# Kernel optimization log

Hardware: AMD Instinct MI355X
Metric: run time of the kernel (lower is better)

Reference implementation:

```python
import jax, jax.numpy as jnp
import numpy as np

NUM_EMBEDDINGS = 8192
EMBEDDING_DIM = 256
PROJECTION_DIM = 128


def setup_inputs() -> dict:
    key = jax.random.key(0)
    k_x, k_cb, k_w, k_b = jax.random.split(key, 4)
    x = jax.random.normal(k_x, (16, 1024, EMBEDDING_DIM), dtype=jnp.float32)
    codebook = jax.random.normal(k_cb, (NUM_EMBEDDINGS, EMBEDDING_DIM), dtype=jnp.float32)
    proj_w = jax.random.normal(k_w, (EMBEDDING_DIM, PROJECTION_DIM), dtype=jnp.float32) / np.sqrt(EMBEDDING_DIM)
    proj_b = jax.random.normal(k_b, (PROJECTION_DIM,), dtype=jnp.float32) * 0.01
    return {"x": x, "codebook": codebook, "proj_w": proj_w, "proj_b": proj_b}


def reference(x, codebook, proj_w, proj_b):
    # Flatten tokens: [N, D]
    x_flat = x.reshape(-1, EMBEDDING_DIM)
    # Project tokens and codebook into the distance space: [N, P], [K, P]
    x_proj = x_flat @ proj_w + proj_b
    cb_proj = codebook @ proj_w + proj_b
    # Squared euclidean distances via expansion: [N, K]
    distances = (
        jnp.sum(x_proj ** 2, axis=1, keepdims=True)
        - 2.0 * (x_proj @ cb_proj.T)
        + jnp.sum(cb_proj ** 2, axis=1)
    )
    idx = jnp.argmin(distances, axis=1)
    discrete = jax.nn.one_hot(idx, NUM_EMBEDDINGS, dtype=x.dtype)  # [N, K]
    # One-hot matmul lookup (disguised gather): [N, D]
    quantized = (discrete @ codebook).reshape(x.shape)
    return (discrete, quantized)
```

## Files before the change

kernel.cpp:

```cpp
#include <hip/hip_runtime.h>
#include <math.h>

#define D 256
#define P 128
#define K 8192
#define NTOK 16384
#define NROWS (NTOK + K)
#define NCHUNK 8
#define KCHUNK (K / NCHUNK)
#define CAPC 128
#define MARGIN 3.0f
#define FLT_BIG 3.402823466e+38f

typedef __attribute__((ext_vector_type(8))) short bf16x8;
typedef __attribute__((ext_vector_type(4))) float f32x4;
typedef __attribute__((ext_vector_type(8))) unsigned short u16x8;

__device__ __forceinline__ unsigned short f32_to_bf16_rne(float f) {
    unsigned int u = __float_as_uint(f);
    u = (u + 0x7fffu + ((u >> 16) & 1u)) >> 16;
    return (unsigned short)u;
}

__global__ __launch_bounds__(256) void zero_kernel(float4* __restrict__ p, size_t n4) {
    size_t i = (size_t)blockIdx.x * blockDim.x + threadIdx.x;
    size_t stride = (size_t)gridDim.x * blockDim.x;
    float4 z; z.x = 0.f; z.y = 0.f; z.z = 0.f; z.w = 0.f;
    for (; i < n4; i += stride) p[i] = z;
}

__global__ __launch_bounds__(256) void proj_kernel(
    const float* __restrict__ x, const float* __restrict__ cb,
    const float* __restrict__ w, const float* __restrict__ bias,
    float* __restrict__ xproj, float* __restrict__ cproj,
    float* __restrict__ xnorm, float* __restrict__ cnorm,
    unsigned short* __restrict__ xh, unsigned short* __restrict__ chs,
    unsigned long long* __restrict__ best, int* __restrict__ cnt)
{
    __shared__ float As[16][D];
    const int tid = threadIdx.x;
    const int row0 = blockIdx.x * 16;

    {
        int g = blockIdx.x * 256 + tid;
        if (g < NTOK) { best[g] = 0xFFFFFFFFFFFFFFFFull; cnt[g] = 0; }
    }

    for (int i = tid; i < 16 * (D / 4); i += 256) {
        int r = i / (D / 4);
        int c4 = i % (D / 4);
        int gr = row0 + r;
        const float* src = (gr < NTOK) ? (x + (size_t)gr * D)
                                       : (cb + (size_t)(gr - NTOK) * D);
        float4 v = ((const float4*)src)[c4];
        ((float4*)&As[r][0])[c4] = v;
    }
    __syncthreads();

    const int r = tid >> 4;
    const int c0 = (tid & 15) * 8;

    float acc[8];
#pragma unroll
    for (int j = 0; j < 8; j++) acc[j] = 0.f;

    for (int d = 0; d < D; d += 4) {
        float4 a4 = *(const float4*)&As[r][d];
#pragma unroll
        for (int dd = 0; dd < 4; dd++) {
            float av = (dd == 0) ? a4.x : (dd == 1) ? a4.y : (dd == 2) ? a4.z : a4.w;
            float4 w0 = *(const float4*)&w[(size_t)(d + dd) * P + c0];
            float4 w1 = *(const float4*)&w[(size_t)(d + dd) * P + c0 + 4];
            acc[0] = fmaf(av, w0.x, acc[0]);
            acc[1] = fmaf(av, w0.y, acc[1]);
            acc[2] = fmaf(av, w0.z, acc[2]);
            acc[3] = fmaf(av, w0.w, acc[3]);
            acc[4] = fmaf(av, w1.x, acc[4]);
            acc[5] = fmaf(av, w1.y, acc[5]);
            acc[6] = fmaf(av, w1.z, acc[6]);
            acc[7] = fmaf(av, w1.w, acc[7]);
        }
    }

    float out[8];
    float nrm = 0.f;
    u16x8 hv;
#pragma unroll
    for (int j = 0; j < 8; j++) {
        out[j] = acc[j] + bias[c0 + j];
        nrm = fmaf(out[j], out[j], nrm);
        hv[j] = f32_to_bf16_rne(out[j]);
    }

    const int gr = row0 + r;
    if (gr < NTOK) {
        float* dst = xproj + (size_t)gr * P;
        float4 o0; o0.x = out[0]; o0.y = out[1]; o0.z = out[2]; o0.w = out[3];
        float4 o1; o1.x = out[4]; o1.y = out[5]; o1.z = out[6]; o1.w = out[7];
        *(float4*)&dst[c0] = o0;
        *(float4*)&dst[c0 + 4] = o1;
        *(u16x8*)(xh + (size_t)gr * P + c0) = hv;
    } else {
        int row = gr - NTOK;
        float* dst = cproj + (size_t)row * P;
        float4 o0; o0.x = out[0]; o0.y = out[1]; o0.z = out[2]; o0.w = out[3];
        float4 o1; o1.x = out[4]; o1.y = out[5]; o1.z = out[6]; o1.w = out[7];
        *(float4*)&dst[c0] = o0;
        *(float4*)&dst[c0 + 4] = o1;
        int t64 = row >> 6, rg = (row >> 4) & 3, l15 = row & 15;
        int ks = c0 >> 5, quad = (c0 >> 3) & 3;
        size_t atom = ((size_t)(t64 * 16 + rg * 4 + ks) * 4 + quad) * 16 + l15;
        *(u16x8*)(chs + atom * 8) = hv;
    }

#pragma unroll
    for (int off = 1; off < 16; off <<= 1)
        nrm += __shfl_xor(nrm, off, 16);
    if ((tid & 15) == 0) {
        if (gr < NTOK) xnorm[gr] = nrm;
        else           cnorm[gr - NTOK] = nrm;
    }
}

__global__ __launch_bounds__(256) void filter_kernel(
    const unsigned short* __restrict__ xh, const unsigned short* __restrict__ chs,
    const float* __restrict__ xnorm, const float* __restrict__ cnorm,
    int* __restrict__ cnt, int* __restrict__ cand)
{
    const int tid = threadIdx.x;
    const int tok0 = blockIdx.x * 128;
    const int k0 = blockIdx.y * KCHUNK;

    const int wave = tid >> 6;
    const int lane = tid & 63;
    const int quad = lane >> 4;
    const int l15 = lane & 15;

    bf16x8 afrag[2][4];
#pragma unroll
    for (int mi = 0; mi < 2; mi++)
#pragma unroll
        for (int ks = 0; ks < 4; ks++)
            afrag[mi][ks] = *(const bf16x8*)(
                xh + (size_t)(tok0 + wave * 32 + mi * 16 + l15) * P + ks * 32 + quad * 8);

    float xnv[2][4];
#pragma unroll
    for (int mi = 0; mi < 2; mi++)
#pragma unroll
        for (int r = 0; r < 4; r++)
            xnv[mi][r] = xnorm[tok0 + wave * 32 + mi * 16 + quad * 4 + r];

    float rmin[2][4];
#pragma unroll
    for (int mi = 0; mi < 2; mi++)
#pragma unroll
        for (int r = 0; r < 4; r++) rmin[mi][r] = FLT_BIG;

    for (int ct = 0; ct < KCHUNK / 64; ct++) {
        const int kt = k0 + ct * 64;
        const int t64 = kt >> 6;

        f32x4 acc[2][4];
#pragma unroll
        for (int mi = 0; mi < 2; mi++)
#pragma unroll
            for (int nj = 0; nj < 4; nj++)
                acc[mi][nj] = (f32x4)(0.f);

#pragma unroll
        for (int ks = 0; ks < 4; ks++) {
            const bf16x8* base = (const bf16x8*)(chs) + (size_t)(t64 * 16 + ks) * 64 + lane;
            bf16x8 b0 = base[0 * 4 * 64];
            bf16x8 b1 = base[1 * 4 * 64];
            bf16x8 b2 = base[2 * 4 * 64];
            bf16x8 b3 = base[3 * 4 * 64];
            acc[0][0] = __builtin_amdgcn_mfma_f32_16x16x32_bf16(afrag[0][ks], b0, acc[0][0], 0, 0, 0);
            acc[0][1] = __builtin_amdgcn_mfma_f32_16x16x32_bf16(afrag[0][ks], b1, acc[0][1], 0, 0, 0);
            acc[0][2] = __builtin_amdgcn_mfma_f32_16x16x32_bf16(afrag[0][ks], b2, acc[0][2], 0, 0, 0);
            acc[0][3] = __builtin_amdgcn_mfma_f32_16x16x32_bf16(afrag[0][ks], b3, acc[0][3], 0, 0, 0);
            acc[1][0] = __builtin_amdgcn_mfma_f32_16x16x32_bf16(afrag[1][ks], b0, acc[1][0], 0, 0, 0);
            acc[1][1] = __builtin_amdgcn_mfma_f32_16x16x32_bf16(afrag[1][ks], b1, acc[1][1], 0, 0, 0);
            acc[1][2] = __builtin_amdgcn_mfma_f32_16x16x32_bf16(afrag[1][ks], b2, acc[1][2], 0, 0, 0);
            acc[1][3] = __builtin_amdgcn_mfma_f32_16x16x32_bf16(afrag[1][ks], b3, acc[1][3], 0, 0, 0);
        }

        float cn[4];
#pragma unroll
        for (int nj = 0; nj < 4; nj++) cn[nj] = cnorm[kt + nj * 16 + l15];

#pragma unroll
        for (int mi = 0; mi < 2; mi++)
#pragma unroll
            for (int r = 0; r < 4; r++) {
                float d[4];
#pragma unroll
                for (int nj = 0; nj < 4; nj++)
                    d[nj] = (xnv[mi][r] - 2.0f * acc[mi][nj][r]) + cn[nj];
                float m = fminf(fminf(d[0], d[1]), fminf(d[2], d[3]));
#pragma unroll
                for (int off = 1; off < 16; off <<= 1)
                    m = fminf(m, __shfl_xor(m, off));
                float rm = fminf(rmin[mi][r], m);
                rmin[mi][r] = rm;
                float thr = rm + MARGIN;
                const int tok = tok0 + wave * 32 + mi * 16 + quad * 4 + r;
#pragma unroll
                for (int nj = 0; nj < 4; nj++) {
                    if (d[nj] <= thr) {
                        int pos = atomicAdd(&cnt[tok], 1);
                        if (pos < CAPC) cand[(size_t)tok * CAPC + pos] = kt + nj * 16 + l15;
                    }
                }
            }
    }
}

__global__ __launch_bounds__(256) void rescore_kernel(
    const float* __restrict__ xproj, const float* __restrict__ cproj,
    const float* __restrict__ xnorm, const float* __restrict__ cnorm,
    const int* __restrict__ cnt, const int* __restrict__ cand,
    unsigned long long* __restrict__ best)
{
    const int tid = threadIdx.x;
    const int lane = tid & 63;
    const int wave = tid >> 6;
    const int t = blockIdx.x * 4 + wave;

    int n = cnt[t];
    if (n > CAPC) n = CAPC;
    const float xn = xnorm[t];
    const float* xr = xproj + (size_t)t * P;

    for (int j = lane; j < n; j += 64) {
        int k = cand[(size_t)t * CAPC + j];
        const float* cr = cproj + (size_t)k * P;
        float s = 0.f;
#pragma unroll 8
        for (int p = 0; p < P; p += 4) {
            float4 a = *(const float4*)&xr[p];
            float4 b = *(const float4*)&cr[p];
            s = fmaf(a.x, b.x, s);
            s = fmaf(a.y, b.y, s);
            s = fmaf(a.z, b.z, s);
            s = fmaf(a.w, b.w, s);
        }
        float dist = (xn - 2.0f * s) + cnorm[k];
        unsigned long long pack =
            ((unsigned long long)__float_as_uint(dist) << 32) |
            (unsigned long long)(unsigned)k;
        atomicMin(&best[t], pack);
    }
}

__global__ __launch_bounds__(256) void finalize_kernel(
    const unsigned long long* __restrict__ best, const float* __restrict__ cb,
    float* __restrict__ discrete, float* __restrict__ quant)
{
    __shared__ int sidx[64];
    const int tid = threadIdx.x;
    const int tok0 = blockIdx.x * 64;

    if (tid < 64) {
        int t = tok0 + tid;
        int bi = (int)(best[t] & 0xFFFFFFFFull);
        sidx[tid] = bi;
        discrete[(size_t)t * K + bi] = 1.0f;
    }
    __syncthreads();

    for (int i = tid; i < 64 * (D / 4); i += 256) {
        int t = i >> 6;
        int c4 = i & 63;
        int bi = sidx[t];
        float4 v = ((const float4*)(cb + (size_t)bi * D))[c4];
        ((float4*)(quant + (size_t)(tok0 + t) * D))[c4] = v;
    }
}

extern "C" void kernel_launch(void* const* d_in, const int* in_sizes, int n_in,
                              void* d_out, int out_size, void* d_ws, size_t ws_size,
                              hipStream_t stream) {
    const float* x    = (const float*)d_in[0];
    const float* cb   = (const float*)d_in[1];
    const float* w    = (const float*)d_in[2];
    const float* bias = (const float*)d_in[3];

    float* out = (float*)d_out;
    float* discrete = out;
    float* quant = out + (size_t)NTOK * K;

    char* ws = (char*)d_ws;
    size_t off = 0;
    float* xproj = (float*)(ws + off); off += (size_t)NTOK * P * 4;
    float* cproj = (float*)(ws + off); off += (size_t)K * P * 4;
    float* xnorm = (float*)(ws + off); off += (size_t)NTOK * 4;
    float* cnorm = (float*)(ws + off); off += (size_t)K * 4;
    unsigned short* xh  = (unsigned short*)(ws + off); off += (size_t)NTOK * P * 2;
    unsigned short* chs = (unsigned short*)(ws + off); off += (size_t)K * P * 2;
    int* cnt  = (int*)(ws + off); off += (size_t)NTOK * 4;
    int* cand = (int*)(ws + off); off += (size_t)NTOK * CAPC * 4;
    unsigned long long* best = (unsigned long long*)(ws + off); off += (size_t)NTOK * 8;

    zero_kernel<<<dim3(8192), dim3(256), 0, stream>>>(
        (float4*)discrete, (size_t)NTOK * K / 4);

    proj_kernel<<<dim3(NROWS / 16), dim3(256), 0, stream>>>(
        x, cb, w, bias, xproj, cproj, xnorm, cnorm, xh, chs, best, cnt);

    filter_kernel<<<dim3(NTOK / 128, NCHUNK), dim3(256), 0, stream>>>(
        xh, chs, xnorm, cnorm, cnt, cand);

    rescore_kernel<<<dim3(NTOK / 4), dim3(256), 0, stream>>>(
        xproj, cproj, xnorm, cnorm, cnt, cand, best);

    finalize_kernel<<<dim3(NTOK / 64), dim3(256), 0, stream>>>(
        best, cb, discrete, quant);
}
```

Baseline: 969.5 us.

## Fuse one-hot zeroing into filter kernel and merge rescore with finalize

```diff
diff --git a/kernel.cpp b/kernel.cpp
--- a/kernel.cpp
+++ b/kernel.cpp
@@ -22,20 +22,13 @@
     return (unsigned short)u;
 }
 
-__global__ __launch_bounds__(256) void zero_kernel(float4* __restrict__ p, size_t n4) {
-    size_t i = (size_t)blockIdx.x * blockDim.x + threadIdx.x;
-    size_t stride = (size_t)gridDim.x * blockDim.x;
-    float4 z; z.x = 0.f; z.y = 0.f; z.z = 0.f; z.w = 0.f;
-    for (; i < n4; i += stride) p[i] = z;
-}
-
 __global__ __launch_bounds__(256) void proj_kernel(
     const float* __restrict__ x, const float* __restrict__ cb,
     const float* __restrict__ w, const float* __restrict__ bias,
     float* __restrict__ xproj, float* __restrict__ cproj,
     float* __restrict__ xnorm, float* __restrict__ cnorm,
     unsigned short* __restrict__ xh, unsigned short* __restrict__ chs,
-    unsigned long long* __restrict__ best, int* __restrict__ cnt)
+    int* __restrict__ cnt)
 {
     __shared__ float As[16][D];
     const int tid = threadIdx.x;
@@ -43,7 +36,7 @@
 
     {
         int g = blockIdx.x * 256 + tid;
-        if (g < NTOK) { best[g] = 0xFFFFFFFFFFFFFFFFull; cnt[g] = 0; }
+        if (g < NTOK) cnt[g] = 0;
     }
 
     for (int i = tid; i < 16 * (D / 4); i += 256) {
@@ -122,20 +115,25 @@
     }
 }
 
-__global__ __launch_bounds__(256) void filter_kernel(
+__global__ __launch_bounds__(256) void filterz_kernel(
     const unsigned short* __restrict__ xh, const unsigned short* __restrict__ chs,
     const float* __restrict__ xnorm, const float* __restrict__ cnorm,
-    int* __restrict__ cnt, int* __restrict__ cand)
+    int* __restrict__ cnt, int* __restrict__ cand,
+    float* __restrict__ discrete)
 {
     const int tid = threadIdx.x;
     const int tok0 = blockIdx.x * 128;
     const int k0 = blockIdx.y * KCHUNK;
+    const int flat = blockIdx.y * gridDim.x + blockIdx.x;
 
     const int wave = tid >> 6;
     const int lane = tid & 63;
     const int quad = lane >> 4;
     const int l15 = lane & 15;
 
+    f32x4* zbase = (f32x4*)discrete + (size_t)flat * 32768;
+    const f32x4 zv = (f32x4)(0.f);
+
     bf16x8 afrag[2][4];
 #pragma unroll
     for (int mi = 0; mi < 2; mi++)
@@ -160,6 +158,10 @@
     for (int ct = 0; ct < KCHUNK / 64; ct++) {
         const int kt = k0 + ct * 64;
         const int t64 = kt >> 6;
+
+#pragma unroll
+        for (int s = 0; s < 8; s++)
+            zbase[(size_t)ct * 2048 + s * 256 + tid] = zv;
 
         f32x4 acc[2][4];
 #pragma unroll
@@ -216,56 +218,56 @@
     }
 }
 
-__global__ __launch_bounds__(256) void rescore_kernel(
+__global__ __launch_bounds__(256) void rescorefinal_kernel(
     const float* __restrict__ xproj, const float* __restrict__ cproj,
     const float* __restrict__ xnorm, const float* __restrict__ cnorm,
     const int* __restrict__ cnt, const int* __restrict__ cand,
-    unsigned long long* __restrict__ best)
-{
-    const int tid = threadIdx.x;
-    const int lane = tid & 63;
-    const int wave = tid >> 6;
-    const int t = blockIdx.x * 4 + wave;
-
-    int n = cnt[t];
-    if (n > CAPC) n = CAPC;
-    const float xn = xnorm[t];
-    const float* xr = xproj + (size_t)t * P;
-
-    for (int j = lane; j < n; j += 64) {
-        int k = cand[(size_t)t * CAPC + j];
-        const float* cr = cproj + (size_t)k * P;
-        float s = 0.f;
-#pragma unroll 8
-        for (int p = 0; p < P; p += 4) {
-            float4 a = *(const float4*)&xr[p];
-            float4 b = *(const float4*)&cr[p];
-            s = fmaf(a.x, b.x, s);
-            s = fmaf(a.y, b.y, s);
-            s = fmaf(a.z, b.z, s);
-            s = fmaf(a.w, b.w, s);
-        }
-        float dist = (xn - 2.0f * s) + cnorm[k];
-        unsigned long long pack =
-            ((unsigned long long)__float_as_uint(dist) << 32) |
-            (unsigned long long)(unsigned)k;
-        atomicMin(&best[t], pack);
-    }
-}
-
-__global__ __launch_bounds__(256) void finalize_kernel(
-    const unsigned long long* __restrict__ best, const float* __restrict__ cb,
+    const float* __restrict__ cb,
     float* __restrict__ discrete, float* __restrict__ quant)
 {
     __shared__ int sidx[64];
     const int tid = threadIdx.x;
+    const int lane = tid & 63;
+    const int wave = tid >> 6;
     const int tok0 = blockIdx.x * 64;
 
-    if (tid < 64) {
-        int t = tok0 + tid;
-        int bi = (int)(best[t] & 0xFFFFFFFFull);
-        sidx[tid] = bi;
-        discrete[(size_t)t * K + bi] = 1.0f;
+    for (int i = 0; i < 16; i++) {
+        const int t = tok0 + wave * 16 + i;
+        int n = cnt[t];
+        if (n > CAPC) n = CAPC;
+        const float xn = xnorm[t];
+        const float* xr = xproj + (size_t)t * P;
+
+        unsigned long long pack = 0xFFFFFFFFFFFFFFFFull;
+        for (int j = lane; j < n; j += 64) {
+            int k = cand[(size_t)t * CAPC + j];
+            const float* cr = cproj + (size_t)k * P;
+            float s = 0.f;
+#pragma unroll 8
+            for (int p = 0; p < P; p += 4) {
+                float4 a = *(const float4*)&xr[p];
+                float4 b = *(const float4*)&cr[p];
+                s = fmaf(a.x, b.x, s);
+                s = fmaf(a.y, b.y, s);
+                s = fmaf(a.z, b.z, s);
+                s = fmaf(a.w, b.w, s);
+            }
+            float dist = (xn - 2.0f * s) + cnorm[k];
+            unsigned long long pk =
+                ((unsigned long long)__float_as_uint(dist) << 32) |
+                (unsigned long long)(unsigned)k;
+            if (pk < pack) pack = pk;
+        }
+#pragma unroll
+        for (int off = 1; off < 64; off <<= 1) {
+            unsigned long long o = __shfl_xor((long long)pack, off);
+            if (o < pack) pack = o;
+        }
+        if (lane == 0) {
+            int bi = (int)(pack & 0xFFFFFFFFull);
+            sidx[wave * 16 + i] = bi;
+            discrete[(size_t)t * K + bi] = 1.0f;
+        }
     }
     __syncthreads();
 
@@ -300,20 +302,13 @@
     unsigned short* chs = (unsigned short*)(ws + off); off += (size_t)K * P * 2;
     int* cnt  = (int*)(ws + off); off += (size_t)NTOK * 4;
     int* cand = (int*)(ws + off); off += (size_t)NTOK * CAPC * 4;
-    unsigned long long* best = (unsigned long long*)(ws + off); off += (size_t)NTOK * 8;
-
-    zero_kernel<<<dim3(8192), dim3(256), 0, stream>>>(
-        (float4*)discrete, (size_t)NTOK * K / 4);
 
     proj_kernel<<<dim3(NROWS / 16), dim3(256), 0, stream>>>(
-        x, cb, w, bias, xproj, cproj, xnorm, cnorm, xh, chs, best, cnt);
-
-    filter_kernel<<<dim3(NTOK / 128, NCHUNK), dim3(256), 0, stream>>>(
-        xh, chs, xnorm, cnorm, cnt, cand);
-
-    rescore_kernel<<<dim3(NTOK / 4), dim3(256), 0, stream>>>(
-        xproj, cproj, xnorm, cnorm, cnt, cand, best);
-
-    finalize_kernel<<<dim3(NTOK / 64), dim3(256), 0, stream>>>(
-        best, cb, discrete, quant);
-}
+        x, cb, w, bias, xproj, cproj, xnorm, cnorm, xh, chs, cnt);
+
+    filterz_kernel<<<dim3(NTOK / 128, NCHUNK), dim3(256), 0, stream>>>(
+        xh, chs, xnorm, cnorm, cnt, cand, discrete);
+
+    rescorefinal_kernel<<<dim3(NTOK / 64), dim3(256), 0, stream>>>(
+        xproj, cproj, xnorm, cnorm, cnt, cand, cb, discrete, quant);
+}
```

Result: faster. 895.5 us (-7.6%).
